# Kernel optimization log

Hardware: AMD Instinct MI355X
Metric: run time of the kernel (lower is better)

The kernel has to match this reference:

```python
import jax, jax.numpy as jnp
import numpy as np

EPS = 1e-12

def l2norm(x, axis):
    # torch.nn.functional.normalize: x / max(||x||_2, eps)
    n = jnp.sqrt(jnp.sum(x * x, axis=axis, keepdims=True))
    return x / jnp.maximum(n, EPS)

def setup_inputs() -> dict:
    key = jax.random.key(0)
    k1, k2, k3, k4 = jax.random.split(key, 4)
    B, Cf, H, W = 128, 1024, 16, 16
    n_att, dv = 312, 300
    img = jax.random.normal(k1, (B, Cf, H, W), dtype=jnp.float32)
    # V is initialized from row-normalized w2v embeddings in the module
    V = l2norm(jax.random.normal(k2, (n_att, dv), dtype=jnp.float32), axis=1)
    W1 = jax.random.normal(k3, (dv, Cf), dtype=jnp.float32)
    W2 = jax.random.normal(k4, (dv, Cf), dtype=jnp.float32)
    return {"img": img, "V": V, "W1": W1, "W2": W2}

def reference(img, V, W1, W2):
    vv = l2norm(V, axis=1)                               # [i, v]
    B, Cf, H, Wd = img.shape
    av = l2norm(img.reshape(B, Cf, H * Wd), axis=1)      # [b, f, r]
    Q = vv @ W1                                          # [i, f]
    A = jnp.einsum('if,bfr->bir', Q, av)                 # attention logits
    A = jax.nn.softmax(A, axis=-1)
    F_p = jnp.einsum('bir,bfr->bif', A, av)              # attended features
    Pred_att = jnp.einsum('if,bif->bi', vv @ W2, F_p)
    return Pred_att
```

## Files before the change

### kernel.cpp

```cpp
#include <hip/hip_runtime.h>
#include <math.h>

#define NB   128
#define CF   1024
#define RR   256
#define NA   312
#define DV   300
#define MT   640
#define NKC  32
#define NQ   160
#define NPI  320
#define ABYTES 40960
#define BBYTES 16384
#define BUFSZ  57344

typedef _Float16 half8  __attribute__((ext_vector_type(8)));
typedef _Float16 half4  __attribute__((ext_vector_type(4)));
typedef float float16v  __attribute__((ext_vector_type(16)));
typedef float float4v   __attribute__((ext_vector_type(4)));

__device__ __forceinline__ void gll16(const void* g, void* l) {
    __builtin_amdgcn_global_load_lds(
        (const __attribute__((address_space(1))) void*)g,
        (__attribute__((address_space(3))) void*)l, 16, 0, 0);
}

__launch_bounds__(256, 4)
__global__ void k_q(const float* __restrict__ V, const float* __restrict__ W1,
                    const float* __restrict__ W2, _Float16* __restrict__ Qb) {
    int ib = blockIdx.x;
    int t  = threadIdx.x;
    bool isQ2 = ib >= 80;
    int i0l = (ib - (isQ2 ? 80 : 0)) * 4;
    __shared__ float inv4[4];
    float acc[4][4];
    #pragma unroll
    for (int ii = 0; ii < 4; ++ii)
        #pragma unroll
        for (int j = 0; j < 4; ++j) acc[ii][j] = 0.f;
    if (i0l < NA) {
        int row = t >> 6, l64 = t & 63;
        float s = 0.f;
        for (int v = l64; v < DV; v += 64) { float x = V[(i0l + row) * DV + v]; s += x * x; }
        #pragma unroll
        for (int o = 32; o; o >>= 1) s += __shfl_xor(s, o, 64);
        if (l64 == 0) inv4[row] = 1.f / fmaxf(sqrtf(s), 1e-12f);
        __syncthreads();
        const float* W  = isQ2 ? W2 : W1;
        const float* Vb = V + (size_t)i0l * DV;
        for (int v = 0; v < DV; v += 2) {
            float4v w0 = *(const float4v*)(W + (size_t)v * CF + t * 4);
            float4v w1 = *(const float4v*)(W + (size_t)(v + 1) * CF + t * 4);
            #pragma unroll
            for (int ii = 0; ii < 4; ++ii) {
                float a0 = Vb[(size_t)ii * DV + v];
                float a1 = Vb[(size_t)ii * DV + v + 1];
                #pragma unroll
                for (int j = 0; j < 4; ++j) acc[ii][j] += a0 * w0[j] + a1 * w1[j];
            }
        }
        #pragma unroll
        for (int ii = 0; ii < 4; ++ii)
            #pragma unroll
            for (int j = 0; j < 4; ++j) acc[ii][j] *= inv4[ii];
    }
    int fg = t >> 3;
    int fo = (t & 7) * 4;
    int q12 = isQ2 ? 1 : 0;
    #pragma unroll
    for (int ii = 0; ii < 4; ++ii) {
        half4 h;
        #pragma unroll
        for (int j = 0; j < 4; ++j) h[j] = (_Float16)acc[ii][j];
        *(half4*)&Qb[((size_t)fg * MT + (2 * (i0l + ii) + q12)) * 32 + fo] = h;
    }
}

extern __shared__ char smem[];
__launch_bounds__(512, 2)
__global__ void k_fused(const float* __restrict__ img, const _Float16* __restrict__ Qb,
                        float* __restrict__ pm, float* __restrict__ ps,
                        float* __restrict__ pd) {
    int lin = blockIdx.x;
    int b   = lin >> 1;
    int rh  = lin & 1;

    int tid  = threadIdx.x;
    int lane = tid & 63;
    int w    = tid >> 6;
    int wm   = w >> 1;
    int wn   = w & 1;
    int nl   = lane & 31;
    int kh   = lane >> 5;

    int aG[5];
    #pragma unroll
    for (int j = 0; j < 5; ++j) {
        int s = tid + j * 512;
        aG[j] = ((s % 640) * 4 + (s / 640)) * 16;
    }
    int bG[2];
    #pragma unroll
    for (int j = 0; j < 2; ++j) {
        int s = tid + j * 512;
        bG[j] = (s >> 5) * (RR * 4) + (s & 31) * 16;
    }
    const char* gA = (const char*)Qb;
    const char* gB = (const char*)img + ((size_t)b * CF * RR + (size_t)rh * 128) * 4;

    float16v acc[5][2];
    #pragma unroll
    for (int i = 0; i < 5; ++i)
        #pragma unroll
        for (int j = 0; j < 2; ++j)
            #pragma unroll
            for (int gi = 0; gi < 16; ++gi) acc[i][j][gi] = 0.f;
    float ssq = 0.f;

    #define STAGE(kc_) do {                                                        \
        int kcl = (kc_) < NKC ? (kc_) : (NKC - 1);                                 \
        char* buf = smem + (((kc_) & 1) ? BUFSZ : 0);                              \
        const char* aS = gA + (size_t)kcl * ABYTES;                                \
        const char* bS = gB + (size_t)kcl * 32768;                                 \
        _Pragma("unroll")                                                          \
        for (int j = 0; j < 5; ++j) gll16(aS + aG[j], buf + (tid + j * 512) * 16); \
        _Pragma("unroll")                                                          \
        for (int j = 0; j < 2; ++j)                                                \
            gll16(bS + bG[j], buf + ABYTES + (tid + j * 512) * 16);                \
    } while (0)

    #define COMPUTE(kc_) do {                                                      \
        char* buf = smem + (((kc_) & 1) ? BUFSZ : 0);                              \
        const char* Al = buf; const char* Bl = buf + ABYTES;                       \
        int c0 = wn * 64 + nl;                                                     \
        _Pragma("unroll")                                                          \
        for (int ks = 0; ks < 2; ++ks) {                                           \
            int kb = ks * 2 + kh;                                                  \
            float bv0[8], bv1[8];                                                  \
            _Pragma("unroll")                                                      \
            for (int j = 0; j < 8; ++j) {                                          \
                bv0[j] = *(const float*)(Bl + (((kb * 8 + j) * 128) + c0) * 4);    \
                bv1[j] = *(const float*)(Bl + (((kb * 8 + j) * 128) + c0 + 32) * 4); \
            }                                                                      \
            half8 bf0, bf1;                                                        \
            _Pragma("unroll")                                                      \
            for (int j = 0; j < 8; ++j) {                                          \
                bf0[j] = (_Float16)bv0[j]; bf1[j] = (_Float16)bv1[j];              \
            }                                                                      \
            _Pragma("unroll")                                                      \
            for (int mt = 0; mt < 5; ++mt) {                                       \
                half8 af = *(const half8*)(Al + ((size_t)kb * 640 + wm * 160 + mt * 32 + nl) * 16); \
                acc[mt][0] = __builtin_amdgcn_mfma_f32_32x32x16_f16(af, bf0, acc[mt][0], 0, 0, 0);  \
                acc[mt][1] = __builtin_amdgcn_mfma_f32_32x32x16_f16(af, bf1, acc[mt][1], 0, 0, 0);  \
            }                                                                      \
        }                                                                          \
    } while (0)

    STAGE(0);
    #pragma unroll 1
    for (int kc = 0; kc < NKC; ++kc) {
        STAGE(kc + 1);
        asm volatile("s_waitcnt vmcnt(7)" ::: "memory");
        __builtin_amdgcn_s_barrier();
        __builtin_amdgcn_sched_barrier(0);
        COMPUTE(kc);
        {
            if (tid < 128) {
                const char* Bl = smem + ((kc & 1) ? BUFSZ : 0) + ABYTES;
                #pragma unroll
                for (int f = 0; f < 32; ++f) {
                    float x = *(const float*)(Bl + (f * 128 + tid) * 4);
                    ssq += x * x;
                }
            }
        }
        __builtin_amdgcn_sched_barrier(0);
        __builtin_amdgcn_s_barrier();
    }
    asm volatile("s_waitcnt vmcnt(0)" ::: "memory");
    __builtin_amdgcn_s_barrier();
    __builtin_amdgcn_sched_barrier(0);
    #undef STAGE
    #undef COMPUTE

    float* ssq_lds = (float*)smem;
    float* mred    = (float*)(smem + 512);
    float* mg      = (float*)(smem + 3072);
    float* sred    = (float*)(smem + 4352);
    float* dred    = (float*)(smem + 6912);

    if (tid < 128) ssq_lds[tid] = ssq;
    __syncthreads();
    int c0 = wn * 64 + nl;
    float iv0 = 1.f / fmaxf(sqrtf(ssq_lds[c0]), 1e-12f);
    float iv1 = 1.f / fmaxf(sqrtf(ssq_lds[c0 + 32]), 1e-12f);
    #pragma unroll
    for (int mt = 0; mt < 5; ++mt)
        #pragma unroll
        for (int gi = 0; gi < 16; ++gi) {
            acc[mt][0][gi] *= iv0;
            acc[mt][1][gi] *= iv1;
        }

    #pragma unroll
    for (int mt = 0; mt < 5; ++mt) {
        #pragma unroll
        for (int e = 0; e < 8; ++e) {
            int g = 2 * e;
            float mx = fmaxf(acc[mt][0][g], acc[mt][1][g]);
            #pragma unroll
            for (int off = 1; off <= 16; off <<= 1)
                mx = fmaxf(mx, __shfl_xor(mx, off, 64));
            if (nl == 0) {
                int row = (g & 3) + 8 * (g >> 2) + 4 * kh;
                mred[wn * NPI + wm * 80 + mt * 16 + (row >> 1)] = mx;
            }
        }
    }
    __syncthreads();
    if (tid < NPI) mg[tid] = fmaxf(mred[tid], mred[NPI + tid]);
    __syncthreads();

    #pragma unroll
    for (int mt = 0; mt < 5; ++mt) {
        #pragma unroll
        for (int e = 0; e < 8; ++e) {
            int g = 2 * e;
            int row = (g & 3) + 8 * (g >> 2) + 4 * kh;
            int i   = wm * 80 + mt * 16 + (row >> 1);
            float m  = mg[i];
            float e0 = __expf(acc[mt][0][g] - m);
            float e1 = __expf(acc[mt][1][g] - m);
            float s = e0 + e1;
            float d = e0 * acc[mt][0][g + 1] + e1 * acc[mt][1][g + 1];
            #pragma unroll
            for (int off = 1; off <= 16; off <<= 1) {
                s += __shfl_xor(s, off, 64);
                d += __shfl_xor(d, off, 64);
            }
            if (nl == 0) {
                sred[wn * NPI + i] = s;
                dred[wn * NPI + i] = d;
            }
        }
    }
    __syncthreads();
    if (tid < NPI) {
        size_t pb = ((size_t)b * 2 + rh) * NPI + tid;
        pm[pb] = mg[tid];
        ps[pb] = sred[tid] + sred[NPI + tid];
        pd[pb] = dred[tid] + dred[NPI + tid];
    }
}

__launch_bounds__(256, 4)
__global__ void k_comb(const float* __restrict__ pm, const float* __restrict__ ps,
                       const float* __restrict__ pd, float* __restrict__ out) {
    int idx = blockIdx.x * 256 + threadIdx.x;
    int b = idx / NPI;
    int i = idx - b * NPI;
    float m0 = pm[(size_t)(b * 2) * NPI + i];
    float m1 = pm[(size_t)(b * 2 + 1) * NPI + i];
    float m  = fmaxf(m0, m1);
    float w0 = __expf(m0 - m), w1 = __expf(m1 - m);
    float s = ps[(size_t)(b * 2) * NPI + i] * w0 + ps[(size_t)(b * 2 + 1) * NPI + i] * w1;
    float d = pd[(size_t)(b * 2) * NPI + i] * w0 + pd[(size_t)(b * 2 + 1) * NPI + i] * w1;
    if (i < NA) out[(size_t)b * NA + i] = d / s;
}

extern "C" void kernel_launch(void* const* d_in, const int* in_sizes, int n_in,
                              void* d_out, int out_size, void* d_ws, size_t ws_size,
                              hipStream_t stream) {
    const float* img = (const float*)d_in[0];
    const float* V   = (const float*)d_in[1];
    const float* W1  = (const float*)d_in[2];
    const float* W2  = (const float*)d_in[3];
    float* out = (float*)d_out;

    char* ws = (char*)d_ws;
    size_t off = 0;
    _Float16* Qb = (_Float16*)(ws + off); off += (size_t)NKC * MT * 32 * 2;
    float*    pm = (float*)(ws + off);    off += (size_t)NB * 2 * NPI * 4;
    float*    ps = (float*)(ws + off);    off += (size_t)NB * 2 * NPI * 4;
    float*    pd = (float*)(ws + off);    off += (size_t)NB * 2 * NPI * 4;

    static bool attr_done = false;
    if (!attr_done) {
        hipFuncSetAttribute((const void*)k_fused,
                            hipFuncAttributeMaxDynamicSharedMemorySize, 2 * BUFSZ);
        attr_done = true;
    }

    k_q<<<dim3(NQ), 256, 0, stream>>>(V, W1, W2, Qb);
    k_fused<<<dim3(256), 512, 2 * BUFSZ, stream>>>(img, Qb, pm, ps, pd);
    k_comb<<<dim3(160), 256, 0, stream>>>(pm, ps, pd, out);
}
```

Measured before the change: 264.3 us.

## Load image tiles through registers, convert to fp16 once, spread ssq across threads

Image tiles are now loaded into registers instead of being copied straight into LDS. Each thread converts its values to fp16 and writes them to LDS in MFMA-ready half8 layout, and accumulates the sum of squares for its slice. This removes the per-wave repeated fp32 LDS reads and conversions inside the MMA loop, and replaces the 128-thread serial ssq pass with work spread over all threads. The loop is restructured into an explicit two-buffer ping-pong with manual waitcnt tuning. The LDS buffer shrinks, at the cost of more register pressure and fragile hand-set vmcnt counts.

```diff
diff --git a/kernel.cpp b/kernel.cpp
--- a/kernel.cpp
+++ b/kernel.cpp
@@ -11,8 +11,8 @@
 #define NQ   160
 #define NPI  320
 #define ABYTES 40960
-#define BBYTES 16384
-#define BUFSZ  57344
+#define BHB    8192
+#define BUFSZ  49152
 
 typedef _Float16 half8  __attribute__((ext_vector_type(8)));
 typedef _Float16 half4  __attribute__((ext_vector_type(4)));
@@ -99,14 +99,10 @@
         int s = tid + j * 512;
         aG[j] = ((s % 640) * 4 + (s / 640)) * 16;
     }
-    int bG[2];
-    #pragma unroll
-    for (int j = 0; j < 2; ++j) {
-        int s = tid + j * 512;
-        bG[j] = (s >> 5) * (RR * 4) + (s & 31) * 16;
-    }
     const char* gA = (const char*)Qb;
-    const char* gB = (const char*)img + ((size_t)b * CF * RR + (size_t)rh * 128) * 4;
+
+    int rB = tid & 127, fq = tid >> 7;
+    const float* gB = img + (size_t)b * CF * RR + (size_t)rh * 128 + rB;
 
     float16v acc[5][2];
     #pragma unroll
@@ -116,37 +112,43 @@
             #pragma unroll
             for (int gi = 0; gi < 16; ++gi) acc[i][j][gi] = 0.f;
     float ssq = 0.f;
-
-    #define STAGE(kc_) do {                                                        \
+    float R0[8], R1[8];
+
+    char* buf0 = smem;
+    char* buf1 = smem + BUFSZ;
+
+    #define BLOAD(kc_, R) do {                                                     \
         int kcl = (kc_) < NKC ? (kc_) : (NKC - 1);                                 \
-        char* buf = smem + (((kc_) & 1) ? BUFSZ : 0);                              \
+        const float* p = gB + ((size_t)kcl * 32 + fq * 8) * RR;                    \
+        _Pragma("unroll")                                                          \
+        for (int j = 0; j < 8; ++j) (R)[j] = p[(size_t)j * RR];                    \
+    } while (0)
+
+    #define AGLL(kc_, buf) do {                                                   \
+        int kcl = (kc_) < NKC ? (kc_) : (NKC - 1);                                 \
         const char* aS = gA + (size_t)kcl * ABYTES;                                \
-        const char* bS = gB + (size_t)kcl * 32768;                                 \
         _Pragma("unroll")                                                          \
-        for (int j = 0; j < 5; ++j) gll16(aS + aG[j], buf + (tid + j * 512) * 16); \
+        for (int j = 0; j < 5; ++j) gll16(aS + aG[j], (buf) + (tid + j * 512) * 16); \
+    } while (0)
+
+    #define CVTW(R, buf) do {                                                      \
+        half8 h;                                                                   \
         _Pragma("unroll")                                                          \
-        for (int j = 0; j < 2; ++j)                                                \
-            gll16(bS + bG[j], buf + ABYTES + (tid + j * 512) * 16);                \
+        for (int j = 0; j < 8; ++j) {                                              \
+            ssq += (R)[j] * (R)[j];                                                \
+            h[j] = (_Float16)(R)[j];                                               \
+        }                                                                          \
+        *(half8*)((buf) + ABYTES + fq * 2048 + rB * 16) = h;                       \
     } while (0)
 
-    #define COMPUTE(kc_) do {                                                      \
-        char* buf = smem + (((kc_) & 1) ? BUFSZ : 0);                              \
-        const char* Al = buf; const char* Bl = buf + ABYTES;                       \
+    #define COMPUTE(buf) do {                                                      \
+        const char* Al = (buf); const char* Bl = (buf) + ABYTES;                   \
         int c0 = wn * 64 + nl;                                                     \
         _Pragma("unroll")                                                          \
         for (int ks = 0; ks < 2; ++ks) {                                           \
             int kb = ks * 2 + kh;                                                  \
-            float bv0[8], bv1[8];                                                  \
-            _Pragma("unroll")                                                      \
-            for (int j = 0; j < 8; ++j) {                                          \
-                bv0[j] = *(const float*)(Bl + (((kb * 8 + j) * 128) + c0) * 4);    \
-                bv1[j] = *(const float*)(Bl + (((kb * 8 + j) * 128) + c0 + 32) * 4); \
-            }                                                                      \
-            half8 bf0, bf1;                                                        \
-            _Pragma("unroll")                                                      \
-            for (int j = 0; j < 8; ++j) {                                          \
-                bf0[j] = (_Float16)bv0[j]; bf1[j] = (_Float16)bv1[j];              \
-            }                                                                      \
+            half8 bf0 = *(const half8*)(Bl + kb * 2048 + c0 * 16);                 \
+            half8 bf1 = *(const half8*)(Bl + kb * 2048 + (c0 + 32) * 16);          \
             _Pragma("unroll")                                                      \
             for (int mt = 0; mt < 5; ++mt) {                                       \
                 half8 af = *(const half8*)(Al + ((size_t)kb * 640 + wm * 160 + mt * 32 + nl) * 16); \
@@ -156,44 +158,67 @@
         }                                                                          \
     } while (0)
 
-    STAGE(0);
-    #pragma unroll 1
-    for (int kc = 0; kc < NKC; ++kc) {
-        STAGE(kc + 1);
-        asm volatile("s_waitcnt vmcnt(7)" ::: "memory");
-        __builtin_amdgcn_s_barrier();
-        __builtin_amdgcn_sched_barrier(0);
-        COMPUTE(kc);
-        {
-            if (tid < 128) {
-                const char* Bl = smem + ((kc & 1) ? BUFSZ : 0) + ABYTES;
-                #pragma unroll
-                for (int f = 0; f < 32; ++f) {
-                    float x = *(const float*)(Bl + (f * 128 + tid) * 4);
-                    ssq += x * x;
-                }
-            }
-        }
-        __builtin_amdgcn_sched_barrier(0);
-        __builtin_amdgcn_s_barrier();
-    }
-    asm volatile("s_waitcnt vmcnt(0)" ::: "memory");
+    BLOAD(0, R0);
+    AGLL(0, buf0);
+    __builtin_amdgcn_sched_barrier(0);
+    CVTW(R0, buf0);
+    BLOAD(1, R1);
+    AGLL(1, buf1);
+    __builtin_amdgcn_sched_barrier(0);
+    asm volatile("s_waitcnt vmcnt(13) lgkmcnt(0)" ::: "memory");
     __builtin_amdgcn_s_barrier();
     __builtin_amdgcn_sched_barrier(0);
-    #undef STAGE
+
+    #pragma unroll 1
+    for (int kc = 0; kc < NKC; kc += 2) {
+        BLOAD(kc + 2, R0);
+        __builtin_amdgcn_sched_barrier(0);
+        COMPUTE(buf0);
+        __builtin_amdgcn_sched_barrier(0);
+        asm volatile("s_waitcnt vmcnt(8)" ::: "memory");
+        CVTW(R1, buf1);
+        asm volatile("s_waitcnt lgkmcnt(0)" ::: "memory");
+        __builtin_amdgcn_s_barrier();
+        __builtin_amdgcn_sched_barrier(0);
+        AGLL(kc + 2, buf0);
+        __builtin_amdgcn_sched_barrier(0);
+
+        BLOAD(kc + 3, R1);
+        __builtin_amdgcn_sched_barrier(0);
+        COMPUTE(buf1);
+        __builtin_amdgcn_sched_barrier(0);
+        asm volatile("s_waitcnt vmcnt(8)" ::: "memory");
+        if (kc + 2 < NKC) CVTW(R0, buf0);
+        asm volatile("s_waitcnt lgkmcnt(0)" ::: "memory");
+        __builtin_amdgcn_s_barrier();
+        __builtin_amdgcn_sched_barrier(0);
+        AGLL(kc + 3, buf1);
+        __builtin_amdgcn_sched_barrier(0);
+    }
+    asm volatile("s_waitcnt vmcnt(0) lgkmcnt(0)" ::: "memory");
+    __builtin_amdgcn_s_barrier();
+    __builtin_amdgcn_sched_barrier(0);
+    #undef BLOAD
+    #undef AGLL
+    #undef CVTW
     #undef COMPUTE
 
     float* ssq_lds = (float*)smem;
-    float* mred    = (float*)(smem + 512);
-    float* mg      = (float*)(smem + 3072);
-    float* sred    = (float*)(smem + 4352);
-    float* dred    = (float*)(smem + 6912);
-
-    if (tid < 128) ssq_lds[tid] = ssq;
+    float* ssq_r   = (float*)(smem + 2048);
+    float* mred    = (float*)(smem + 2560);
+    float* mg      = (float*)(smem + 5120);
+    float* sred    = (float*)(smem + 6400);
+    float* dred    = (float*)(smem + 8960);
+
+    ssq_lds[tid] = ssq;
+    __syncthreads();
+    if (tid < 128)
+        ssq_r[tid] = ssq_lds[tid] + ssq_lds[tid + 128] +
+                     ssq_lds[tid + 256] + ssq_lds[tid + 384];
     __syncthreads();
     int c0 = wn * 64 + nl;
-    float iv0 = 1.f / fmaxf(sqrtf(ssq_lds[c0]), 1e-12f);
-    float iv1 = 1.f / fmaxf(sqrtf(ssq_lds[c0 + 32]), 1e-12f);
+    float iv0 = 1.f / fmaxf(sqrtf(ssq_r[c0]), 1e-12f);
+    float iv1 = 1.f / fmaxf(sqrtf(ssq_r[c0 + 32]), 1e-12f);
     #pragma unroll
     for (int mt = 0; mt < 5; ++mt)
         #pragma unroll
```

Result: slower. 275.6 us (+4.3%).

## Load image tiles directly to registers, keep only Q in LDS

Applied to the files above, without the earlier changes.

The image operand is no longer staged through LDS with global_load_lds. Each lane now loads its own B column values straight into registers one chunk ahead and converts them to f16 in registers. The sum-of-squares for the column norms is taken from those registers and reduced with a single lane shuffle, which removes the separate tid<128 LDS pass and one barrier per iteration. LDS use drops to two Q buffers and MFMA sections get raised priority. The cost is more VGPRs for the prefetch registers and uncoalesced-ish strided global loads, which may hurt occupancy or memory efficiency.

```diff
diff --git a/kernel.cpp b/kernel.cpp
--- a/kernel.cpp
+++ b/kernel.cpp
@@ -11,8 +11,6 @@
 #define NQ   160
 #define NPI  320
 #define ABYTES 40960
-#define BBYTES 16384
-#define BUFSZ  57344
 
 typedef _Float16 half8  __attribute__((ext_vector_type(8)));
 typedef _Float16 half4  __attribute__((ext_vector_type(4)));
@@ -99,14 +97,11 @@
         int s = tid + j * 512;
         aG[j] = ((s % 640) * 4 + (s / 640)) * 16;
     }
-    int bG[2];
-    #pragma unroll
-    for (int j = 0; j < 2; ++j) {
-        int s = tid + j * 512;
-        bG[j] = (s >> 5) * (RR * 4) + (s & 31) * 16;
-    }
     const char* gA = (const char*)Qb;
-    const char* gB = (const char*)img + ((size_t)b * CF * RR + (size_t)rh * 128) * 4;
+
+    int c_lo = wn * 64 + nl;
+    const float* pB = img + (size_t)b * CF * RR + (size_t)rh * 128 + c_lo
+                      + (size_t)kh * 8 * RR;
 
     float16v acc[5][2];
     #pragma unroll
@@ -115,85 +110,94 @@
         for (int j = 0; j < 2; ++j)
             #pragma unroll
             for (int gi = 0; gi < 16; ++gi) acc[i][j][gi] = 0.f;
-    float ssq = 0.f;
-
-    #define STAGE(kc_) do {                                                        \
+    float ssq0 = 0.f, ssq1 = 0.f;
+    float Bv0[2][8], Bv1[2][8];
+    half8 bf0[2], bf1[2];
+
+    #define AGLL(kc_, bsel) do {                                                   \
         int kcl = (kc_) < NKC ? (kc_) : (NKC - 1);                                 \
-        char* buf = smem + (((kc_) & 1) ? BUFSZ : 0);                              \
         const char* aS = gA + (size_t)kcl * ABYTES;                                \
-        const char* bS = gB + (size_t)kcl * 32768;                                 \
+        char* buf_ = smem + (size_t)(bsel) * ABYTES;                               \
         _Pragma("unroll")                                                          \
-        for (int j = 0; j < 5; ++j) gll16(aS + aG[j], buf + (tid + j * 512) * 16); \
+        for (int j = 0; j < 5; ++j) gll16(aS + aG[j], buf_ + (tid + j * 512) * 16); \
+    } while (0)
+
+    #define BLOAD(kc_) do {                                                        \
+        int kcl = (kc_) < NKC ? (kc_) : (NKC - 1);                                 \
+        const float* p = pB + (size_t)kcl * 32 * RR;                               \
         _Pragma("unroll")                                                          \
-        for (int j = 0; j < 2; ++j)                                                \
-            gll16(bS + bG[j], buf + ABYTES + (tid + j * 512) * 16);                \
+        for (int ks = 0; ks < 2; ++ks)                                             \
+            _Pragma("unroll")                                                      \
+            for (int j = 0; j < 8; ++j) {                                          \
+                Bv0[ks][j] = p[(size_t)(ks * 16 + j) * RR];                        \
+                Bv1[ks][j] = p[(size_t)(ks * 16 + j) * RR + 32];                   \
+            }                                                                      \
     } while (0)
 
-    #define COMPUTE(kc_) do {                                                      \
-        char* buf = smem + (((kc_) & 1) ? BUFSZ : 0);                              \
-        const char* Al = buf; const char* Bl = buf + ABYTES;                       \
-        int c0 = wn * 64 + nl;                                                     \
+    #define BCVT() do {                                                            \
+        _Pragma("unroll")                                                          \
+        for (int ks = 0; ks < 2; ++ks)                                             \
+            _Pragma("unroll")                                                      \
+            for (int j = 0; j < 8; ++j) {                                          \
+                float x0 = Bv0[ks][j], x1 = Bv1[ks][j];                            \
+                ssq0 += x0 * x0; ssq1 += x1 * x1;                                  \
+                bf0[ks][j] = (_Float16)x0; bf1[ks][j] = (_Float16)x1;              \
+            }                                                                      \
+    } while (0)
+
+    #define COMPUTE(bsel) do {                                                     \
+        const char* Al = smem + (size_t)(bsel) * ABYTES;                           \
         _Pragma("unroll")                                                          \
         for (int ks = 0; ks < 2; ++ks) {                                           \
             int kb = ks * 2 + kh;                                                  \
-            float bv0[8], bv1[8];                                                  \
-            _Pragma("unroll")                                                      \
-            for (int j = 0; j < 8; ++j) {                                          \
-                bv0[j] = *(const float*)(Bl + (((kb * 8 + j) * 128) + c0) * 4);    \
-                bv1[j] = *(const float*)(Bl + (((kb * 8 + j) * 128) + c0 + 32) * 4); \
-            }                                                                      \
-            half8 bf0, bf1;                                                        \
-            _Pragma("unroll")                                                      \
-            for (int j = 0; j < 8; ++j) {                                          \
-                bf0[j] = (_Float16)bv0[j]; bf1[j] = (_Float16)bv1[j];              \
-            }                                                                      \
             _Pragma("unroll")                                                      \
             for (int mt = 0; mt < 5; ++mt) {                                       \
                 half8 af = *(const half8*)(Al + ((size_t)kb * 640 + wm * 160 + mt * 32 + nl) * 16); \
-                acc[mt][0] = __builtin_amdgcn_mfma_f32_32x32x16_f16(af, bf0, acc[mt][0], 0, 0, 0);  \
-                acc[mt][1] = __builtin_amdgcn_mfma_f32_32x32x16_f16(af, bf1, acc[mt][1], 0, 0, 0);  \
+                acc[mt][0] = __builtin_amdgcn_mfma_f32_32x32x16_f16(af, bf0[ks], acc[mt][0], 0, 0, 0); \
+                acc[mt][1] = __builtin_amdgcn_mfma_f32_32x32x16_f16(af, bf1[ks], acc[mt][1], 0, 0, 0); \
             }                                                                      \
         }                                                                          \
     } while (0)
 
-    STAGE(0);
+    AGLL(0, 0);
+    BLOAD(0);
+    asm volatile("s_waitcnt vmcnt(32)" ::: "memory");
+    __builtin_amdgcn_s_barrier();
+    AGLL(1, 1);
+    __builtin_amdgcn_sched_barrier(0);
+
     #pragma unroll 1
     for (int kc = 0; kc < NKC; ++kc) {
-        STAGE(kc + 1);
-        asm volatile("s_waitcnt vmcnt(7)" ::: "memory");
+        asm volatile("s_waitcnt vmcnt(5)" ::: "memory");
+        BCVT();
+        BLOAD(kc + 1);
+        __builtin_amdgcn_sched_barrier(0);
+        __builtin_amdgcn_s_setprio(1);
+        COMPUTE(kc & 1);
+        __builtin_amdgcn_s_setprio(0);
+        __builtin_amdgcn_sched_barrier(0);
+        asm volatile("s_waitcnt vmcnt(32)" ::: "memory");
         __builtin_amdgcn_s_barrier();
+        AGLL(kc + 2, kc & 1);
         __builtin_amdgcn_sched_barrier(0);
-        COMPUTE(kc);
-        {
-            if (tid < 128) {
-                const char* Bl = smem + ((kc & 1) ? BUFSZ : 0) + ABYTES;
-                #pragma unroll
-                for (int f = 0; f < 32; ++f) {
-                    float x = *(const float*)(Bl + (f * 128 + tid) * 4);
-                    ssq += x * x;
-                }
-            }
-        }
-        __builtin_amdgcn_sched_barrier(0);
-        __builtin_amdgcn_s_barrier();
-    }
-    asm volatile("s_waitcnt vmcnt(0)" ::: "memory");
+    }
+    asm volatile("s_waitcnt vmcnt(0) lgkmcnt(0)" ::: "memory");
     __builtin_amdgcn_s_barrier();
     __builtin_amdgcn_sched_barrier(0);
-    #undef STAGE
+    #undef AGLL
+    #undef BLOAD
+    #undef BCVT
     #undef COMPUTE
 
-    float* ssq_lds = (float*)smem;
-    float* mred    = (float*)(smem + 512);
-    float* mg      = (float*)(smem + 3072);
-    float* sred    = (float*)(smem + 4352);
-    float* dred    = (float*)(smem + 6912);
-
-    if (tid < 128) ssq_lds[tid] = ssq;
-    __syncthreads();
-    int c0 = wn * 64 + nl;
-    float iv0 = 1.f / fmaxf(sqrtf(ssq_lds[c0]), 1e-12f);
-    float iv1 = 1.f / fmaxf(sqrtf(ssq_lds[c0 + 32]), 1e-12f);
+    float* mred = (float*)smem;
+    float* mg   = (float*)(smem + 2560);
+    float* sred = (float*)(smem + 3840);
+    float* dred = (float*)(smem + 6400);
+
+    ssq0 += __shfl_xor(ssq0, 32, 64);
+    ssq1 += __shfl_xor(ssq1, 32, 64);
+    float iv0 = 1.f / fmaxf(sqrtf(ssq0), 1e-12f);
+    float iv1 = 1.f / fmaxf(sqrtf(ssq1), 1e-12f);
     #pragma unroll
     for (int mt = 0; mt < 5; ++mt)
         #pragma unroll
@@ -286,12 +290,12 @@
 
     static bool attr_done = false;
     if (!attr_done) {
-        hipFuncSetAttribute((const void*)k_fused,
-                            hipFuncAttributeMaxDynamicSharedMemorySize, 2 * BUFSZ);
+        (void)hipFuncSetAttribute((const void*)k_fused,
+                                  hipFuncAttributeMaxDynamicSharedMemorySize, 2 * ABYTES);
         attr_done = true;
     }
 
     k_q<<<dim3(NQ), 256, 0, stream>>>(V, W1, W2, Qb);
-    k_fused<<<dim3(256), 512, 2 * BUFSZ, stream>>>(img, Qb, pm, ps, pd);
+    k_fused<<<dim3(256), 512, 2 * ABYTES, stream>>>(img, Qb, pm, ps, pd);
     k_comb<<<dim3(160), 256, 0, stream>>>(pm, ps, pd, out);
 }
```

Measured after the change: 273.4 us. 1.03x slower.
